# Performance work log

Hardware: AMD Instinct MI355X
Metric: run time of the kernel (lower is better)

The kernel has to match this reference:

```python
import jax, jax.numpy as jnp
import numpy as np

B, T, C = 4, 2048, 1024
H, D = 16, 64  # num_heads, head_dim
WINDOW = 256


def setup_inputs() -> dict:
    key = jax.random.key(0)
    k_x, k_qkv, k_proj, k_qb, k_pb = jax.random.split(key, 5)
    x = jax.random.normal(k_x, (B, T, C), dtype=jnp.float32)
    # xavier-uniform-ish init for qkv weight (as in _reset_parameters)
    lim_qkv = float(np.sqrt(6.0 / (C + 3 * C)))
    qkv_w = jax.random.uniform(k_qkv, (3 * C, C), minval=-lim_qkv, maxval=lim_qkv, dtype=jnp.float32)
    qkv_b = jax.random.normal(k_qb, (3 * C,), dtype=jnp.float32) * 0.02
    lim_p = float(np.sqrt(1.0 / C))
    proj_w = jax.random.uniform(k_proj, (C, C), minval=-lim_p, maxval=lim_p, dtype=jnp.float32)
    proj_b = jax.random.normal(k_pb, (C,), dtype=jnp.float32) * 0.02
    # windowed causal mask: attend to j iff j <= i and i - j < WINDOW
    i = jnp.arange(T)[:, None]
    j = jnp.arange(T)[None, :]
    attn_mask = (j <= i) & (i - j < WINDOW)  # [T, T] bool
    return {"x": x, "attn_mask": attn_mask, "qkv_w": qkv_w, "qkv_b": qkv_b,
            "proj_w": proj_w, "proj_b": proj_b}


def reference(x, attn_mask, qkv_w, qkv_b, proj_w, proj_b):
    qkv = (x @ qkv_w.T + qkv_b).reshape(B, T, 3, H, D)
    qkv = jnp.transpose(qkv, (2, 0, 3, 1, 4))
    q, k, v = qkv[0], qkv[1], qkv[2]
    scale = 1.0 / jnp.sqrt(jnp.asarray(D, dtype=q.dtype))
    scores = jnp.einsum('bhqd,bhkd->bhqk', q, k) * scale  # [B,H,T,T]
    neg = jnp.asarray(jnp.finfo(scores.dtype).min, dtype=scores.dtype)
    scores = jnp.where(attn_mask[None, None], scores, neg)
    attn = jax.nn.softmax(scores, axis=-1)
    out = jnp.einsum('bhqk,bhkd->bhqd', attn, v)  # [B,H,T,D]
    out = jnp.transpose(out, (0, 2, 1, 3)).reshape(B, T, C)
    out = out @ proj_w.T + proj_b
    return out
```

## Files before the change

kernel.cpp:

```cpp
#include <hip/hip_runtime.h>

#define BB 4
#define TT 2048
#define CC 1024
#define HH 16
#define DD 64
#define WIN 256

typedef __attribute__((ext_vector_type(8))) short short8;
typedef __attribute__((ext_vector_type(4))) float floatx4;
typedef unsigned short u16;

typedef __attribute__((address_space(3))) void lds_void;
typedef const __attribute__((address_space(1))) void g_void;

__device__ __forceinline__ void gl_lds16(const u16* g, u16* l) {
    __builtin_amdgcn_global_load_lds((g_void*)g, (lds_void*)l, 16, 0, 0);
}

__device__ __forceinline__ float bf2f(u16 u) {
    union { unsigned int i; float f; } v; v.i = ((unsigned int)u) << 16; return v.f;
}
__device__ __forceinline__ u16 f2bf(float f) {
    union { float f; unsigned int i; } v; v.f = f;
    unsigned int x = v.i;
    x += ((x >> 16) & 1u) + 0x7FFFu;
    return (u16)(x >> 16);
}

__global__ void cvt_all(const float* __restrict__ x, const float* __restrict__ qw,
                        const float* __restrict__ pw,
                        u16* __restrict__ xb, u16* __restrict__ wb, u16* __restrict__ pwb) {
    int bid = blockIdx.x;
    const float* src; u16* dst; int off;
    if (bid < 4096)      { src = x;  dst = xb;  off = bid; }
    else if (bid < 5632) { src = qw; dst = wb;  off = bid - 4096; }
    else                 { src = pw; dst = pwb; off = bid - 5632; }
    int i = (off * 256 + (int)threadIdx.x) * 8;
    float4 a = *(const float4*)(src + i);
    float4 b = *(const float4*)(src + i + 4);
    u16 o[8] = { f2bf(a.x), f2bf(a.y), f2bf(a.z), f2bf(a.w),
                 f2bf(b.x), f2bf(b.y), f2bf(b.z), f2bf(b.w) };
    *(uint4*)(dst + i) = *(const uint4*)o;
}

#define VM2()  asm volatile("s_waitcnt vmcnt(2)" ::: "memory")
#define BARX() do { asm volatile("" ::: "memory");                           \
        __builtin_amdgcn_s_barrier();                                        \
        asm volatile("" ::: "memory"); } while (0)

template<int NR>
__device__ __forceinline__ void gemm_core(
    const u16* __restrict__ Amat, const u16* __restrict__ Bw,
    int bM, int bN, u16* lA, u16* lB, floatx4 (&acc)[4][NR])
{
    const int K = CC;
    const int tid = threadIdx.x;
    const int wave = tid >> 6, lane = tid & 63;
    const int wm = wave >> 2, wn = wave & 3;
    const int quad = lane >> 4, l15 = lane & 15;

    const u16* gA[2]; int dA[2];
#pragma unroll
    for (int j = 0; j < 2; ++j) {
        int off = j * 8192 + tid * 16;
        int kh  = off >> 13;
        int o2  = off & 8191;
        int row = (o2 >> 10) * 16 + ((o2 & 1023) >> 6);
        int c   = ((o2 >> 4) & 3) ^ ((row >> 1) & 3);
        gA[j] = Amat + (size_t)(bM + row) * K + kh * 32 + c * 8;
        dA[j] = off >> 1;
    }
    const u16* gB[NR]; int dB[NR];
#pragma unroll
    for (int j = 0; j < NR; ++j) {
        int off = j * 8192 + tid * 16;
        int kh  = (off >= NR * 4096) ? 1 : 0;
        int o2  = off - kh * NR * 4096;
        int row = (o2 >> 10) * 16 + ((o2 & 1023) >> 6);
        int c   = ((o2 >> 4) & 3) ^ ((row >> 1) & 3);
        gB[j] = Bw + (size_t)(bN + row) * K + kh * 32 + c * 8;
        dB[j] = off >> 1;
    }

    const int rdoff = l15 * 32 + ((quad ^ ((l15 >> 1) & 3)) * 8);

    short8 af[4], bf[NR];

    auto stgA = [&](int buf, int t) {
#pragma unroll
        for (int j = 0; j < 2; ++j)
            gl_lds16(gA[j] + t * 64, lA + buf * 8192 + dA[j]);
    };
    auto stgB = [&](int buf, int t) {
#pragma unroll
        for (int j = 0; j < NR; ++j)
            gl_lds16(gB[j] + t * 64, lB + buf * (NR * 4096) + dB[j]);
    };
    auto lda = [&](int buf, int kh) {
#pragma unroll
        for (int i = 0; i < 4; ++i)
            af[i] = *(const short8*)&lA[buf * 8192 + kh * 4096 + (wm * 4 + i) * 512 + rdoff];
    };
    auto ldb = [&](int buf, int kh) {
#pragma unroll
        for (int j = 0; j < NR; ++j)
            bf[j] = *(const short8*)&lB[buf * (NR * 4096) + kh * (NR * 2048) + (wn * NR + j) * 512 + rdoff];
    };
    auto mm = [&]() {
        __builtin_amdgcn_s_setprio(1);
#pragma unroll
        for (int i = 0; i < 4; ++i)
#pragma unroll
            for (int j = 0; j < NR; ++j)
                acc[i][j] = __builtin_amdgcn_mfma_f32_16x16x32_bf16(af[i], bf[j], acc[i][j], 0, 0, 0);
        __builtin_amdgcn_s_setprio(0);
    };

    stgA(0, 0); stgB(0, 0);

    for (int ii = 0; ii < 8; ++ii) {
        const int t1 = 2 * ii + 1;
        const int t2 = (ii < 7) ? 2 * ii + 2 : 15;
        stgA(1, t1); VM2(); BARX();
        lda(0, 0); ldb(0, 0); mm();
        stgB(1, t1);
        lda(0, 1); ldb(0, 1); mm();
        BARX();
        stgA(0, t2); VM2(); BARX();
        lda(1, 0); ldb(1, 0); mm();
        stgB(0, t2);
        lda(1, 1); ldb(1, 1); mm();
        BARX();
    }
}

__global__ __launch_bounds__(512, 4) void gemm_qkv(
    const u16* __restrict__ Amat, const u16* __restrict__ Bw,
    const float* __restrict__ bias,
    u16* __restrict__ Qb, u16* __restrict__ Kb, u16* __restrict__ Vb)
{
    __shared__ u16 lA[2 * 8192];
    __shared__ u16 lB[2 * 12288];
    const int raw = blockIdx.x;
    const int xcd = raw & 7;
    const int l   = raw >> 3;
    const int bM  = (xcd * 8 + (l & 7)) * 128;
    const int bN  = (l >> 3) * 192;

    floatx4 acc[4][3] = {};
    gemm_core<3>(Amat, Bw, bM, bN, lA, lB, acc);

    const int tid = threadIdx.x;
    const int wave = tid >> 6, lane = tid & 63;
    const int wm = wave >> 2, wn = wave & 3;
    const int quad = lane >> 4, l15 = lane & 15;

#pragma unroll
    for (int mf = 0; mf < 4; ++mf)
#pragma unroll
        for (int nf = 0; nf < 3; ++nf) {
            int col = bN + wn * 48 + nf * 16 + l15;
            float bv = bias[col];
            int which = col >> 10, rem = col & 1023;
            int h = rem >> 6, d = rem & 63;
            u16* dst = which == 0 ? Qb : (which == 1 ? Kb : Vb);
#pragma unroll
            for (int rg = 0; rg < 4; ++rg) {
                int row = bM + wm * 64 + mf * 16 + quad * 4 + rg;
                int b = row >> 11, t = row & 2047;
                float v = acc[mf][nf][rg] + bv;
                dst[(((size_t)(b * HH + h)) * TT + t) * DD + d] = f2bf(v);
            }
        }
}

__global__ __launch_bounds__(512, 4) void gemm_proj(
    const u16* __restrict__ Amat, const u16* __restrict__ Bw,
    const float* __restrict__ bias, float* __restrict__ Out)
{
    __shared__ u16 lA[2 * 8192];
    __shared__ u16 lB[2 * 8192];
    const int raw = blockIdx.x;
    const int xcd = raw & 7;
    const int l   = raw >> 3;
    const int bM  = (xcd * 8 + (l & 7)) * 128;
    const int bN  = (l >> 3) * 128;

    floatx4 acc[4][2] = {};
    gemm_core<2>(Amat, Bw, bM, bN, lA, lB, acc);

    const int tid = threadIdx.x;
    const int wave = tid >> 6, lane = tid & 63;
    const int wm = wave >> 2, wn = wave & 3;
    const int quad = lane >> 4, l15 = lane & 15;

#pragma unroll
    for (int mf = 0; mf < 4; ++mf)
#pragma unroll
        for (int nf = 0; nf < 2; ++nf) {
            int col = bN + wn * 32 + nf * 16 + l15;
            float bv = bias[col];
#pragma unroll
            for (int rg = 0; rg < 4; ++rg) {
                int row = bM + wm * 64 + mf * 16 + quad * 4 + rg;
                Out[(size_t)row * CC + col] = acc[mf][nf][rg] + bv;
            }
        }
}

__global__ __launch_bounds__(256) void attn_mfma(
    const u16* __restrict__ Qb, const u16* __restrict__ Kb, const u16* __restrict__ Vb,
    u16* __restrict__ Y)
{
    __shared__ u16 Ks[64][72];
    __shared__ u16 Vt[64][72];
    __shared__ u16 Ps[4][16][72];

    const int tid = threadIdx.x;
    const int wave = tid >> 6, lane = tid & 63;
    const int quad = lane >> 4, l15 = lane & 15;
    const int q0 = blockIdx.y * 64;
    const int bh = blockIdx.x;
    const int b = bh >> 4, h = bh & 15;
    const u16* Qp = Qb + (size_t)bh * TT * DD;
    const u16* Kp = Kb + (size_t)bh * TT * DD;
    const u16* Vp = Vb + (size_t)bh * TT * DD;
    const int qw = q0 + wave * 16;

    short8 qf[2];
    qf[0] = *(const short8*)&Qp[(size_t)(qw + l15) * DD + quad * 8];
    qf[1] = *(const short8*)&Qp[(size_t)(qw + l15) * DD + 32 + quad * 8];

    float m_i[4] = { -1e30f, -1e30f, -1e30f, -1e30f };
    float l_i[4] = { 0.f, 0.f, 0.f, 0.f };
    floatx4 Oacc[4] = {};

    const int kb = (q0 >= WIN) ? (q0 - WIN) : 0;
    for (int j0 = kb; j0 < q0 + 64; j0 += 64) {
        __syncthreads();
#pragma unroll
        for (int it = 0; it < 2; ++it) {
            int slot = tid + it * 256;
            int j = slot >> 3, c8 = (slot & 7) << 3;
            *(uint4*)&Ks[j][c8] = *(const uint4*)&Kp[(size_t)(j0 + j) * DD + c8];
        }
#pragma unroll
        for (int it = 0; it < 2; ++it) {
            int slot = tid + it * 256;
            int j = slot >> 3, d0 = (slot & 7) << 3;
            uint4 raw = *(const uint4*)&Vp[(size_t)(j0 + j) * DD + d0];
            const u16* u = (const u16*)&raw;
#pragma unroll
            for (int i = 0; i < 8; ++i) {
                int d = d0 + i;
                int col = (((j >> 3) ^ (d >> 3)) << 3) + (j & 7);
                Vt[d][col] = u[i];
            }
        }
        __syncthreads();

        floatx4 Sacc[4] = {};
        __builtin_amdgcn_s_setprio(1);
#pragma unroll
        for (int nt = 0; nt < 4; ++nt) {
            short8 kf0 = *(const short8*)&Ks[nt * 16 + l15][quad * 8];
            short8 kf1 = *(const short8*)&Ks[nt * 16 + l15][32 + quad * 8];
            Sacc[nt] = __builtin_amdgcn_mfma_f32_16x16x32_bf16(qf[0], kf0, Sacc[nt], 0, 0, 0);
            Sacc[nt] = __builtin_amdgcn_mfma_f32_16x16x32_bf16(qf[1], kf1, Sacc[nt], 0, 0, 0);
        }
        __builtin_amdgcn_s_setprio(0);

        float mc[4] = { -1e30f, -1e30f, -1e30f, -1e30f };
#pragma unroll
        for (int nt = 0; nt < 4; ++nt)
#pragma unroll
            for (int r = 0; r < 4; ++r) {
                int q = qw + quad * 4 + r;
                int j = j0 + nt * 16 + l15;
                float s = (j <= q && (q - j) < WIN) ? Sacc[nt][r] * 0.125f : -1e30f;
                Sacc[nt][r] = s;
                mc[r] = fmaxf(mc[r], s);
            }
#pragma unroll
        for (int m = 1; m < 16; m <<= 1)
#pragma unroll
            for (int r = 0; r < 4; ++r) mc[r] = fmaxf(mc[r], __shfl_xor(mc[r], m, 64));

        float alpha[4];
#pragma unroll
        for (int r = 0; r < 4; ++r) {
            float mn = fmaxf(m_i[r], mc[r]);
            alpha[r] = __expf(m_i[r] - mn);
            m_i[r] = mn;
        }
        float rs[4] = { 0.f, 0.f, 0.f, 0.f };
#pragma unroll
        for (int nt = 0; nt < 4; ++nt)
#pragma unroll
            for (int r = 0; r < 4; ++r) {
                float s = Sacc[nt][r];
                float p = (s > -1e29f) ? __expf(s - m_i[r]) : 0.f;
                Sacc[nt][r] = p;
                rs[r] += p;
            }
#pragma unroll
        for (int m = 1; m < 16; m <<= 1)
#pragma unroll
            for (int r = 0; r < 4; ++r) rs[r] += __shfl_xor(rs[r], m, 64);
#pragma unroll
        for (int r = 0; r < 4; ++r) l_i[r] = l_i[r] * alpha[r] + rs[r];
#pragma unroll
        for (int dt = 0; dt < 4; ++dt)
#pragma unroll
            for (int r = 0; r < 4; ++r) Oacc[dt][r] *= alpha[r];

#pragma unroll
        for (int nt = 0; nt < 4; ++nt)
#pragma unroll
            for (int r = 0; r < 4; ++r)
                Ps[wave][quad * 4 + r][nt * 16 + l15] = f2bf(Sacc[nt][r]);

        __builtin_amdgcn_s_setprio(1);
#pragma unroll
        for (int ks = 0; ks < 2; ++ks) {
            short8 pf = *(const short8*)&Ps[wave][l15][ks * 32 + quad * 8];
#pragma unroll
            for (int dt = 0; dt < 4; ++dt) {
                int d = dt * 16 + l15;
                int col = (((ks * 4 + quad) ^ (d >> 3)) << 3);
                short8 vf = *(const short8*)&Vt[d][col];
                Oacc[dt] = __builtin_amdgcn_mfma_f32_16x16x32_bf16(pf, vf, Oacc[dt], 0, 0, 0);
            }
        }
        __builtin_amdgcn_s_setprio(0);
    }

    float inv[4];
#pragma unroll
    for (int r = 0; r < 4; ++r) inv[r] = 1.f / l_i[r];
#pragma unroll
    for (int dt = 0; dt < 4; ++dt)
#pragma unroll
        for (int r = 0; r < 4; ++r) {
            int t = qw + quad * 4 + r;
            int d = dt * 16 + l15;
            Y[((size_t)b * TT + t) * CC + h * DD + d] = f2bf(Oacc[dt][r] * inv[r]);
        }
}

extern "C" void kernel_launch(void* const* d_in, const int* in_sizes, int n_in,
                              void* d_out, int out_size, void* d_ws, size_t ws_size,
                              hipStream_t stream) {
    const float* x      = (const float*)d_in[0];
    const float* qkv_w  = (const float*)d_in[2];
    const float* qkv_b  = (const float*)d_in[3];
    const float* proj_w = (const float*)d_in[4];
    const float* proj_b = (const float*)d_in[5];
    float* out = (float*)d_out;

    u16* xb  = (u16*)d_ws;
    u16* wb  = xb  + (size_t)8192 * 1024;
    u16* pwb = wb  + (size_t)3072 * 1024;
    u16* Qb  = pwb + (size_t)1024 * 1024;
    u16* Kb  = Qb  + (size_t)64 * 2048 * 64;
    u16* Vb  = Kb  + (size_t)64 * 2048 * 64;
    u16* Yb  = Vb  + (size_t)64 * 2048 * 64;

    cvt_all<<<6144, 256, 0, stream>>>(x, qkv_w, proj_w, xb, wb, pwb);
    gemm_qkv<<<1024, 512, 0, stream>>>(xb, wb, qkv_b, Qb, Kb, Vb);
    attn_mfma<<<dim3(BB * HH, TT / 64), 256, 0, stream>>>(Qb, Kb, Vb, Yb);
    gemm_proj<<<512, 512, 0, stream>>>(Yb, pwb, proj_b, out);
}
```

Baseline: 219.7 us.

## Widen attention blocks to 128 queries and skip masking/rescale on full tiles

The attention kernel now uses 8 waves per block covering 128 query rows, so each K/V tile loaded into LDS is shared by twice as many waves and the grid is halved. Tiles that lie entirely inside the causal window skip per-element mask evaluation and the -1e29 check. When no row max changes across the whole wave, the alpha exp and the output rescale are skipped. In exchange, each block iterates over more key tiles, including some fully masked for the earlier waves, and has higher per-block LDS and register pressure.

```diff
diff --git a/kernel.cpp b/kernel.cpp
--- a/kernel.cpp
+++ b/kernel.cpp
@@ -209,18 +209,18 @@
         }
 }
 
-__global__ __launch_bounds__(256) void attn_mfma(
+__global__ __launch_bounds__(512) void attn_mfma(
     const u16* __restrict__ Qb, const u16* __restrict__ Kb, const u16* __restrict__ Vb,
     u16* __restrict__ Y)
 {
     __shared__ u16 Ks[64][72];
     __shared__ u16 Vt[64][72];
-    __shared__ u16 Ps[4][16][72];
+    __shared__ u16 Ps[8][16][72];
 
     const int tid = threadIdx.x;
     const int wave = tid >> 6, lane = tid & 63;
     const int quad = lane >> 4, l15 = lane & 15;
-    const int q0 = blockIdx.y * 64;
+    const int q0 = blockIdx.y * 128;
     const int bh = blockIdx.x;
     const int b = bh >> 4, h = bh & 15;
     const u16* Qp = Qb + (size_t)bh * TT * DD;
@@ -237,18 +237,14 @@
     floatx4 Oacc[4] = {};
 
     const int kb = (q0 >= WIN) ? (q0 - WIN) : 0;
-    for (int j0 = kb; j0 < q0 + 64; j0 += 64) {
+    for (int j0 = kb; j0 < q0 + 128; j0 += 64) {
         __syncthreads();
-#pragma unroll
-        for (int it = 0; it < 2; ++it) {
-            int slot = tid + it * 256;
-            int j = slot >> 3, c8 = (slot & 7) << 3;
+        {
+            int j = tid >> 3, c8 = (tid & 7) << 3;
             *(uint4*)&Ks[j][c8] = *(const uint4*)&Kp[(size_t)(j0 + j) * DD + c8];
         }
-#pragma unroll
-        for (int it = 0; it < 2; ++it) {
-            int slot = tid + it * 256;
-            int j = slot >> 3, d0 = (slot & 7) << 3;
+        {
+            int j = tid >> 3, d0 = (tid & 7) << 3;
             uint4 raw = *(const uint4*)&Vp[(size_t)(j0 + j) * DD + d0];
             const u16* u = (const u16*)&raw;
 #pragma unroll
@@ -271,49 +267,85 @@
         }
         __builtin_amdgcn_s_setprio(0);
 
+        const bool fullvalid = (j0 + 63 <= qw) && (qw + 15 - j0 <= WIN - 1);
         float mc[4] = { -1e30f, -1e30f, -1e30f, -1e30f };
-#pragma unroll
-        for (int nt = 0; nt < 4; ++nt)
-#pragma unroll
-            for (int r = 0; r < 4; ++r) {
-                int q = qw + quad * 4 + r;
-                int j = j0 + nt * 16 + l15;
-                float s = (j <= q && (q - j) < WIN) ? Sacc[nt][r] * 0.125f : -1e30f;
-                Sacc[nt][r] = s;
-                mc[r] = fmaxf(mc[r], s);
-            }
+        if (fullvalid) {
+#pragma unroll
+            for (int nt = 0; nt < 4; ++nt)
+#pragma unroll
+                for (int r = 0; r < 4; ++r) {
+                    float s = Sacc[nt][r] * 0.125f;
+                    Sacc[nt][r] = s;
+                    mc[r] = fmaxf(mc[r], s);
+                }
+        } else {
+#pragma unroll
+            for (int nt = 0; nt < 4; ++nt)
+#pragma unroll
+                for (int r = 0; r < 4; ++r) {
+                    int q = qw + quad * 4 + r;
+                    int j = j0 + nt * 16 + l15;
+                    float s = (j <= q && (q - j) < WIN) ? Sacc[nt][r] * 0.125f : -1e30f;
+                    Sacc[nt][r] = s;
+                    mc[r] = fmaxf(mc[r], s);
+                }
+        }
 #pragma unroll
         for (int m = 1; m < 16; m <<= 1)
 #pragma unroll
             for (int r = 0; r < 4; ++r) mc[r] = fmaxf(mc[r], __shfl_xor(mc[r], m, 64));
 
+        float mn[4]; bool nor = true;
+#pragma unroll
+        for (int r = 0; r < 4; ++r) {
+            mn[r] = fmaxf(m_i[r], mc[r]);
+            nor = nor && (mn[r] == m_i[r]);
+        }
+        const bool skip = __all(nor);
         float alpha[4];
-#pragma unroll
-        for (int r = 0; r < 4; ++r) {
-            float mn = fmaxf(m_i[r], mc[r]);
-            alpha[r] = __expf(m_i[r] - mn);
-            m_i[r] = mn;
-        }
+        if (!skip) {
+#pragma unroll
+            for (int r = 0; r < 4; ++r) alpha[r] = __expf(m_i[r] - mn[r]);
+        }
+#pragma unroll
+        for (int r = 0; r < 4; ++r) m_i[r] = mn[r];
+
         float rs[4] = { 0.f, 0.f, 0.f, 0.f };
-#pragma unroll
-        for (int nt = 0; nt < 4; ++nt)
-#pragma unroll
-            for (int r = 0; r < 4; ++r) {
-                float s = Sacc[nt][r];
-                float p = (s > -1e29f) ? __expf(s - m_i[r]) : 0.f;
-                Sacc[nt][r] = p;
-                rs[r] += p;
-            }
+        if (fullvalid) {
+#pragma unroll
+            for (int nt = 0; nt < 4; ++nt)
+#pragma unroll
+                for (int r = 0; r < 4; ++r) {
+                    float p = __expf(Sacc[nt][r] - m_i[r]);
+                    Sacc[nt][r] = p;
+                    rs[r] += p;
+                }
+        } else {
+#pragma unroll
+            for (int nt = 0; nt < 4; ++nt)
+#pragma unroll
+                for (int r = 0; r < 4; ++r) {
+                    float s = Sacc[nt][r];
+                    float p = (s > -1e29f) ? __expf(s - m_i[r]) : 0.f;
+                    Sacc[nt][r] = p;
+                    rs[r] += p;
+                }
+        }
 #pragma unroll
         for (int m = 1; m < 16; m <<= 1)
 #pragma unroll
             for (int r = 0; r < 4; ++r) rs[r] += __shfl_xor(rs[r], m, 64);
-#pragma unroll
-        for (int r = 0; r < 4; ++r) l_i[r] = l_i[r] * alpha[r] + rs[r];
-#pragma unroll
-        for (int dt = 0; dt < 4; ++dt)
-#pragma unroll
-            for (int r = 0; r < 4; ++r) Oacc[dt][r] *= alpha[r];
+        if (skip) {
+#pragma unroll
+            for (int r = 0; r < 4; ++r) l_i[r] += rs[r];
+        } else {
+#pragma unroll
+            for (int r = 0; r < 4; ++r) l_i[r] = l_i[r] * alpha[r] + rs[r];
+#pragma unroll
+            for (int dt = 0; dt < 4; ++dt)
+#pragma unroll
+                for (int r = 0; r < 4; ++r) Oacc[dt][r] *= alpha[r];
+        }
 
 #pragma unroll
         for (int nt = 0; nt < 4; ++nt)
@@ -369,6 +401,6 @@
 
     cvt_all<<<6144, 256, 0, stream>>>(x, qkv_w, proj_w, xb, wb, pwb);
     gemm_qkv<<<1024, 512, 0, stream>>>(xb, wb, qkv_b, Qb, Kb, Vb);
-    attn_mfma<<<dim3(BB * HH, TT / 64), 256, 0, stream>>>(Qb, Kb, Vb, Yb);
+    attn_mfma<<<dim3(BB * HH, TT / 128), 512, 0, stream>>>(Qb, Kb, Vb, Yb);
     gemm_proj<<<512, 512, 0, stream>>>(Yb, pwb, proj_b, out);
 }
```

Measured after the change: 231.0 us. 1.05x slower.

## Inline proj GEMM with smaller K-tiles to raise occupancy

Applied to the files above, without the earlier changes.

Replaces the shared gemm_core call in the output projection with an inline loop over K-tiles of 32 instead of 64. This halves the LDS buffers and raises launch_bounds min-blocks from 4 to 8 to allow more resident workgroups. It also keeps a swizzled LDS layout and adds setprio around the MFMAs. The trade-off is twice as many barriers and load stages per K, and the last iteration redundantly re-stages a tile.

```diff
diff --git a/kernel.cpp b/kernel.cpp
--- a/kernel.cpp
+++ b/kernel.cpp
@@ -175,26 +175,70 @@
         }
 }
 
-__global__ __launch_bounds__(512, 4) void gemm_proj(
+__global__ __launch_bounds__(512, 8) void gemm_proj(
     const u16* __restrict__ Amat, const u16* __restrict__ Bw,
     const float* __restrict__ bias, float* __restrict__ Out)
 {
-    __shared__ u16 lA[2 * 8192];
-    __shared__ u16 lB[2 * 8192];
+    const int K = CC;
+    __shared__ u16 lA[2 * 4096];
+    __shared__ u16 lB[2 * 4096];
     const int raw = blockIdx.x;
     const int xcd = raw & 7;
     const int l   = raw >> 3;
     const int bM  = (xcd * 8 + (l & 7)) * 128;
     const int bN  = (l >> 3) * 128;
 
-    floatx4 acc[4][2] = {};
-    gemm_core<2>(Amat, Bw, bM, bN, lA, lB, acc);
-
     const int tid = threadIdx.x;
     const int wave = tid >> 6, lane = tid & 63;
     const int wm = wave >> 2, wn = wave & 3;
     const int quad = lane >> 4, l15 = lane & 15;
 
+    const int off = tid * 16;
+    const int row = (off >> 10) * 16 + ((off & 1023) >> 6);
+    const int c   = ((off >> 4) & 3) ^ ((row >> 1) & 3);
+    const u16* gA0 = Amat + (size_t)(bM + row) * K + c * 8;
+    const u16* gB0 = Bw + (size_t)(bN + row) * K + c * 8;
+    const int d0 = off >> 1;
+
+    const int rdoff = l15 * 32 + ((quad ^ ((l15 >> 1) & 3)) * 8);
+
+    floatx4 acc[4][2] = {};
+    short8 af[4], bf[2];
+
+    auto stg = [&](int buf, int t) {
+        gl_lds16(gA0 + t * 32, lA + buf * 4096 + d0);
+        gl_lds16(gB0 + t * 32, lB + buf * 4096 + d0);
+    };
+    auto ld = [&](int buf) {
+#pragma unroll
+        for (int i = 0; i < 4; ++i)
+            af[i] = *(const short8*)&lA[buf * 4096 + (wm * 4 + i) * 512 + rdoff];
+#pragma unroll
+        for (int j = 0; j < 2; ++j)
+            bf[j] = *(const short8*)&lB[buf * 4096 + (wn * 2 + j) * 512 + rdoff];
+    };
+    auto mm = [&]() {
+        __builtin_amdgcn_s_setprio(1);
+#pragma unroll
+        for (int i = 0; i < 4; ++i)
+#pragma unroll
+            for (int j = 0; j < 2; ++j)
+                acc[i][j] = __builtin_amdgcn_mfma_f32_16x16x32_bf16(af[i], bf[j], acc[i][j], 0, 0, 0);
+        __builtin_amdgcn_s_setprio(0);
+    };
+
+    stg(0, 0);
+    for (int ii = 0; ii < 16; ++ii) {
+        const int t1 = 2 * ii + 1;
+        const int t2 = (ii < 15) ? 2 * ii + 2 : 31;
+        stg(1, t1); VM2(); BARX();
+        ld(0); mm();
+        BARX();
+        stg(0, t2); VM2(); BARX();
+        ld(1); mm();
+        BARX();
+    }
+
 #pragma unroll
     for (int mf = 0; mf < 4; ++mf)
 #pragma unroll
@@ -203,8 +247,8 @@
             float bv = bias[col];
 #pragma unroll
             for (int rg = 0; rg < 4; ++rg) {
-                int row = bM + wm * 64 + mf * 16 + quad * 4 + rg;
-                Out[(size_t)row * CC + col] = acc[mf][nf][rg] + bv;
+                int rw = bM + wm * 64 + mf * 16 + quad * 4 + rg;
+                Out[(size_t)rw * CC + col] = acc[mf][nf][rg] + bv;
             }
         }
 }
```

Result: slower. 244.4 us (+11.2%).
